# Performance work log

Hardware: AMD Instinct MI355X
Metric: run time of the kernel (lower is better)

Reference implementation:

```python
import jax, jax.numpy as jnp
import numpy as np


def setup_inputs() -> dict:
    key = jax.random.key(0)
    ks = jax.random.split(key, 7)
    B, T, U = 8, 200, 50
    D_enc, D_dec, J, V = 512, 512, 512, 1024
    s = 0.05
    return {
        "h_enc": jax.random.normal(ks[0], (B, T, 1, D_enc), dtype=jnp.float32),
        "h_dec": jax.random.normal(ks[1], (B, 1, U, D_dec), dtype=jnp.float32),
        "W_enc": jax.random.normal(ks[2], (J, D_enc), dtype=jnp.float32) * s,
        "b_enc": jax.random.normal(ks[3], (J,), dtype=jnp.float32) * s,
        "W_dec": jax.random.normal(ks[4], (J, D_dec), dtype=jnp.float32) * s,
        "W_out": jax.random.normal(ks[5], (V, J), dtype=jnp.float32) * s,
        "b_out": jax.random.normal(ks[6], (V,), dtype=jnp.float32) * s,
    }


def reference(h_enc, h_dec, W_enc, b_enc, W_dec, W_out, b_out):
    # lin_enc: (B,T,1,D_enc) -> (B,T,1,J) ; lin_dec (no bias): (B,1,U,D_dec) -> (B,1,U,J)
    e = jnp.einsum("btod,jd->btoj", h_enc, W_enc) + b_enc
    d = jnp.einsum("boud,jd->bouj", h_dec, W_dec)
    # broadcast add -> (B,T,U,J), Tanh activation
    z = jnp.tanh(e + d)
    # lin_out: (B,T,U,J) -> (B,T,U,V)
    return jnp.einsum("btuj,vj->btuv", z, W_out) + b_out
```

## Files before the change

kernel.cpp:

```cpp
#include <hip/hip_runtime.h>
#include <hip/hip_bf16.h>


typedef short bf16x8 __attribute__((ext_vector_type(8)));
typedef float fx4 __attribute__((ext_vector_type(4)));

static constexpr int KD = 512;
static constexpr int V = 1024;

__device__ inline unsigned short f2bf(float f) {
    union { float f; unsigned u; } v; v.f = f;
    unsigned r = v.u + 0x7fffu + ((v.u >> 16) & 1u);
    return (unsigned short)(r >> 16);
}
__device__ inline float bf2f(unsigned short h) {
    union { float f; unsigned u; } v; v.u = ((unsigned)h) << 16; return v.f;
}
__device__ inline float fast_tanh(float x) {
    float p = __builtin_amdgcn_exp2f(x * 2.885390081777926f);
    return 1.0f - 2.0f * __builtin_amdgcn_rcpf(p + 1.0f);
}
__device__ inline void gld_lds16(const void* g, void* l) {
    __builtin_amdgcn_global_load_lds(
        (const __attribute__((address_space(1))) void*)g,
        (__attribute__((address_space(3))) void*)l, 16, 0, 0);
}

__global__ __launch_bounds__(256) void prep(
    const float* __restrict__ h_enc, const float* __restrict__ W_enc,
    const float* __restrict__ b_enc, const float* __restrict__ h_dec,
    const float* __restrict__ W_dec, const float* __restrict__ W_out,
    float* __restrict__ e, float* __restrict__ dd, unsigned short* __restrict__ Wb) {
    const int bx = blockIdx.x;
    const int t = threadIdx.x;
    if (bx >= 256) {
        int i = ((bx - 256) * 256 + t) * 8;
        fx4 a = *(const fx4*)(W_out + i);
        fx4 b = *(const fx4*)(W_out + i + 4);
        unsigned short p[8];
        #pragma unroll
        for (int j = 0; j < 4; j++) { p[j] = f2bf(a[j]); p[j + 4] = f2bf(b[j]); }
        *(bf16x8*)(Wb + i) = *(bf16x8*)p;
        return;
    }
    const float* A; const float* W; const float* bias; float* out;
    int Mrows, mb, nb;
    if (bx < 200) { A = h_enc; W = W_enc; bias = b_enc; out = e;  Mrows = 1600; mb = bx >> 3; nb = bx & 7; }
    else { int b2 = bx - 200; A = h_dec; W = W_dec; bias = nullptr; out = dd; Mrows = 400; mb = b2 >> 3; nb = b2 & 7; }

    __shared__ unsigned short As[64 * 32];
    __shared__ unsigned short Ws[64 * 32];
    const int lane = t & 63, wid = t >> 6;
    const int m0 = mb * 64, n0 = nb * 64;
    const int wm = (wid & 1) * 32, wn = (wid >> 1) * 32;

    fx4 acc[2][2];
    const fx4 z4 = {0.f, 0.f, 0.f, 0.f};
    acc[0][0] = z4; acc[0][1] = z4; acc[1][0] = z4; acc[1][1] = z4;

    const int sr = t >> 2;
    const int skc = (t & 3) * 8;
    const int ar = (m0 + sr < Mrows) ? (m0 + sr) : (Mrows - 1);
    const float* Ap = A + (size_t)ar * KD + skc;
    const float* Wp = W + (size_t)(n0 + sr) * KD + skc;
    unsigned short* asl = &As[sr * 32 + skc];
    unsigned short* wsl = &Ws[sr * 32 + skc];

    for (int ph = 0; ph < 2; ph++) {
        const int wmode = (ph == 1);
        for (int kb = 0; kb < 16; kb++) {
            const int k0 = kb * 32;
            fx4 a0 = *(const fx4*)(Ap + k0);
            fx4 a1 = *(const fx4*)(Ap + k0 + 4);
            fx4 w0 = *(const fx4*)(Wp + k0);
            fx4 w1 = *(const fx4*)(Wp + k0 + 4);
            unsigned short pa[8], pw[8];
            #pragma unroll
            for (int i = 0; i < 4; i++) {
                unsigned short h;
                pa[i] = f2bf(a0[i]); pa[i + 4] = f2bf(a1[i]);
                h = f2bf(w0[i]); pw[i]     = wmode ? f2bf(w0[i] - bf2f(h)) : h;
                h = f2bf(w1[i]); pw[i + 4] = wmode ? f2bf(w1[i] - bf2f(h)) : h;
            }
            *(bf16x8*)asl = *(bf16x8*)pa;
            *(bf16x8*)wsl = *(bf16x8*)pw;
            __syncthreads();
            bf16x8 af[2], wf[2];
            #pragma unroll
            for (int f = 0; f < 2; f++) {
                af[f] = *(const bf16x8*)&As[(wm + f * 16 + (lane & 15)) * 32 + (lane >> 4) * 8];
                wf[f] = *(const bf16x8*)&Ws[(wn + f * 16 + (lane & 15)) * 32 + (lane >> 4) * 8];
            }
            #pragma unroll
            for (int fm = 0; fm < 2; fm++)
                #pragma unroll
                for (int fn = 0; fn < 2; fn++)
                    acc[fm][fn] = __builtin_amdgcn_mfma_f32_16x16x32_bf16(
                        af[fm], wf[fn], acc[fm][fn], 0, 0, 0);
            __syncthreads();
        }
    }
    const int colb = n0 + wn + (lane & 15);
    const int rowb = m0 + wm + (lane >> 4) * 4;
    float bo[2];
    bo[0] = bias ? bias[colb] : 0.f;
    bo[1] = bias ? bias[colb + 16] : 0.f;
    #pragma unroll
    for (int fm = 0; fm < 2; fm++) {
        #pragma unroll
        for (int r = 0; r < 4; r++) {
            int row = rowb + fm * 16 + r;
            if (row < Mrows) {
                float* op = out + (size_t)row * KD;
                op[colb] = acc[fm][0][r] + bo[0];
                op[colb + 16] = acc[fm][1][r] + bo[1];
            }
        }
    }
}

__global__ __launch_bounds__(256) void tanh_z(
    const float* __restrict__ e, const float* __restrict__ d,
    unsigned short* __restrict__ Z) {
    const int t = threadIdx.x;
    const int m = blockIdx.x * 4 + (t >> 6);
    const int kc = (t & 63) * 8;
    const int bt = m / 50;
    const int u = m - bt * 50;
    const int b = m / 10000;
    const float* ep = e + (size_t)bt * KD + kc;
    const float* dp = d + (size_t)(b * 50 + u) * KD + kc;
    fx4 e0 = *(const fx4*)ep, e1 = *(const fx4*)(ep + 4);
    fx4 d0 = *(const fx4*)dp, d1 = *(const fx4*)(dp + 4);
    unsigned short p[8];
    #pragma unroll
    for (int i = 0; i < 4; i++) {
        p[i] = f2bf(fast_tanh(e0[i] + d0[i]));
        p[i + 4] = f2bf(fast_tanh(e1[i] + d1[i]));
    }
    *(bf16x8*)(Z + (size_t)m * KD + kc) = *(bf16x8*)p;
}

__global__ __launch_bounds__(512, 2) void gemm_out_k8(
    const unsigned short* __restrict__ Z, const unsigned short* __restrict__ Wb,
    const float* __restrict__ b_out, float* __restrict__ out) {
    __shared__ unsigned short As[2][2][256 * 32];
    __shared__ unsigned short Bs[2][2][256 * 32];
    const int t = threadIdx.x;
    const int lane = t & 63, wid = t >> 6;
    const int bid = blockIdx.x;
    const int n0 = (bid & 3) * 256;
    const int m0 = (bid >> 2) * 256;
    const int wm = (wid >> 2) * 128;
    const int wn = (wid & 3) * 64;

    fx4 acc[8][4];
    const fx4 z4 = {0.f, 0.f, 0.f, 0.f};
    #pragma unroll
    for (int i = 0; i < 8; i++)
        #pragma unroll
        for (int j = 0; j < 4; j++) acc[i][j] = z4;

    size_t gA[2], gB[2];
    int lb[2];
    #pragma unroll
    for (int q = 0; q < 2; q++) {
        int rl = (wid * 2 + q) * 16 + (lane >> 2);
        int kc = (lane & 3) * 8;
        int ra = m0 + rl; if (ra > 79999) ra = 79999;
        gA[q] = (size_t)ra * KD + kc;
        gB[q] = (size_t)(n0 + rl) * KD + kc;
        lb[q] = (wid * 2 + q) * 512;
    }

    const int offA = (wm + (lane & 15)) * 32 + (lane >> 4) * 8;
    const int offB = (wn + (lane & 15)) * 32 + (lane >> 4) * 8;

    gld_lds16(Z + gA[0], &As[0][0][lb[0]]);
    gld_lds16(Z + gA[1], &As[0][0][lb[1]]);
    gld_lds16(Wb + gB[0], &Bs[0][0][lb[0]]);
    gld_lds16(Wb + gB[1], &Bs[0][0][lb[1]]);
    gld_lds16(Z + gA[0] + 32, &As[0][1][lb[0]]);
    gld_lds16(Z + gA[1] + 32, &As[0][1][lb[1]]);
    gld_lds16(Wb + gB[0] + 32, &Bs[0][1][lb[0]]);
    gld_lds16(Wb + gB[1] + 32, &Bs[0][1][lb[1]]);
    asm volatile("s_waitcnt vmcnt(4)" ::: "memory");
    __builtin_amdgcn_s_barrier();

    #pragma unroll 2
    for (int kt = 0; kt < 8; kt++) {
        const int cb = kt & 1, cb2 = cb ^ 1;
        const size_t ko = (size_t)(kt + 1) * 64;
        const bool pf = (kt < 7);
        bf16x8 afA[4], afB[4], bfA[4];

        #pragma unroll
        for (int i = 0; i < 4; i++) afA[i] = *(const bf16x8*)&As[cb][0][offA + i * 512];
        #pragma unroll
        for (int i = 0; i < 4; i++) bfA[i] = *(const bf16x8*)&Bs[cb][0][offB + i * 512];
        if (pf) {
            gld_lds16(Z + gA[0] + ko, &As[cb2][0][lb[0]]);
            gld_lds16(Z + gA[1] + ko, &As[cb2][0][lb[1]]);
        }
        __builtin_amdgcn_s_barrier();
        asm volatile("s_waitcnt lgkmcnt(0)" ::: "memory");
        __builtin_amdgcn_sched_barrier(0);
        __builtin_amdgcn_s_setprio(1);
        #pragma unroll
        for (int m = 0; m < 4; m++)
            #pragma unroll
            for (int n = 0; n < 4; n++)
                acc[m][n] = __builtin_amdgcn_mfma_f32_16x16x32_bf16(afA[m], bfA[n], acc[m][n], 0, 0, 0);
        __builtin_amdgcn_s_setprio(0);
        __builtin_amdgcn_s_barrier();

        #pragma unroll
        for (int i = 0; i < 4; i++) afB[i] = *(const bf16x8*)&As[cb][0][offA + (4 + i) * 512];
        if (pf) {
            gld_lds16(Wb + gB[0] + ko, &Bs[cb2][0][lb[0]]);
            gld_lds16(Wb + gB[1] + ko, &Bs[cb2][0][lb[1]]);
            asm volatile("s_waitcnt vmcnt(4)" ::: "memory");
        } else {
            asm volatile("s_waitcnt vmcnt(0)" ::: "memory");
        }
        __builtin_amdgcn_s_barrier();
        asm volatile("s_waitcnt lgkmcnt(0)" ::: "memory");
        __builtin_amdgcn_sched_barrier(0);
        __builtin_amdgcn_s_setprio(1);
        #pragma unroll
        for (int m = 0; m < 4; m++)
            #pragma unroll
            for (int n = 0; n < 4; n++)
                acc[4 + m][n] = __builtin_amdgcn_mfma_f32_16x16x32_bf16(afB[m], bfA[n], acc[4 + m][n], 0, 0, 0);
        __builtin_amdgcn_s_setprio(0);
        __builtin_amdgcn_s_barrier();

        #pragma unroll
        for (int i = 0; i < 4; i++) afA[i] = *(const bf16x8*)&As[cb][1][offA + i * 512];
        #pragma unroll
        for (int i = 0; i < 4; i++) bfA[i] = *(const bf16x8*)&Bs[cb][1][offB + i * 512];
        if (pf) {
            gld_lds16(Z + gA[0] + ko + 32, &As[cb2][1][lb[0]]);
            gld_lds16(Z + gA[1] + ko + 32, &As[cb2][1][lb[1]]);
        }
        __builtin_amdgcn_s_barrier();
        asm volatile("s_waitcnt lgkmcnt(0)" ::: "memory");
        __builtin_amdgcn_sched_barrier(0);
        __builtin_amdgcn_s_setprio(1);
        #pragma unroll
        for (int m = 0; m < 4; m++)
            #pragma unroll
            for (int n = 0; n < 4; n++)
                acc[m][n] = __builtin_amdgcn_mfma_f32_16x16x32_bf16(afA[m], bfA[n], acc[m][n], 0, 0, 0);
        __builtin_amdgcn_s_setprio(0);
        __builtin_amdgcn_s_barrier();

        #pragma unroll
        for (int i = 0; i < 4; i++) afB[i] = *(const bf16x8*)&As[cb][1][offA + (4 + i) * 512];
        if (pf) {
            gld_lds16(Wb + gB[0] + ko + 32, &Bs[cb2][1][lb[0]]);
            gld_lds16(Wb + gB[1] + ko + 32, &Bs[cb2][1][lb[1]]);
            asm volatile("s_waitcnt vmcnt(4)" ::: "memory");
        }
        __builtin_amdgcn_s_barrier();
        asm volatile("s_waitcnt lgkmcnt(0)" ::: "memory");
        __builtin_amdgcn_sched_barrier(0);
        __builtin_amdgcn_s_setprio(1);
        #pragma unroll
        for (int m = 0; m < 4; m++)
            #pragma unroll
            for (int n = 0; n < 4; n++)
                acc[4 + m][n] = __builtin_amdgcn_mfma_f32_16x16x32_bf16(afB[m], bfA[n], acc[4 + m][n], 0, 0, 0);
        __builtin_amdgcn_s_setprio(0);
        __builtin_amdgcn_s_barrier();
    }

    const int colb = n0 + wn + (lane & 15);
    const int rowb = m0 + wm + (lane >> 4) * 4;
    float bo[4];
    #pragma unroll
    for (int fn = 0; fn < 4; fn++) bo[fn] = b_out[colb + fn * 16];
    #pragma unroll
    for (int fm = 0; fm < 8; fm++) {
        #pragma unroll
        for (int r = 0; r < 4; r++) {
            const int row = rowb + fm * 16 + r;
            if (row < 80000) {
                float* op = out + (size_t)row * V;
                #pragma unroll
                for (int fn = 0; fn < 4; fn++)
                    op[colb + fn * 16] = acc[fm][fn][r] + bo[fn];
            }
        }
    }
}

extern "C" void kernel_launch(void* const* d_in, const int* in_sizes, int n_in,
                              void* d_out, int out_size, void* d_ws, size_t ws_size,
                              hipStream_t stream) {
    const float* h_enc = (const float*)d_in[0];
    const float* h_dec = (const float*)d_in[1];
    const float* W_enc = (const float*)d_in[2];
    const float* b_enc = (const float*)d_in[3];
    const float* W_dec = (const float*)d_in[4];
    const float* W_out = (const float*)d_in[5];
    const float* b_out = (const float*)d_in[6];
    float* out = (float*)d_out;

    float* e = (float*)d_ws;
    float* dd = e + 1600 * KD;
    unsigned short* Wb = (unsigned short*)(dd + 400 * KD);
    unsigned short* Zb = Wb + (size_t)V * KD;

    prep<<<512, 256, 0, stream>>>(h_enc, W_enc, b_enc, h_dec, W_dec, W_out, e, dd, Wb);
    tanh_z<<<20000, 256, 0, stream>>>(e, dd, Zb);
    gemm_out_k8<<<313 * 4, 512, 0, stream>>>(Zb, Wb, b_out, out);
}
```

Measured before the change: 455.0 us.

## Fuse tanh(e+d) activation into output GEMM A-tile loading

Removes the separate tanh_z kernel and its bf16 Z intermediate. The GEMM now loads fp32 e and d rows into registers, computes tanh, converts to bf16 and writes the A tile into LDS itself, while W_out tiles still use direct global-to-LDS loads. This avoids the Z write and reread traffic and one launch. In exchange, tanh is recomputed once per N-block (4x), and it adds VALU and register pressure inside the MFMA pipeline.

```diff
diff --git a/kernel.cpp b/kernel.cpp
--- a/kernel.cpp
+++ b/kernel.cpp
@@ -119,30 +119,9 @@
     }
 }
 
-__global__ __launch_bounds__(256) void tanh_z(
-    const float* __restrict__ e, const float* __restrict__ d,
-    unsigned short* __restrict__ Z) {
-    const int t = threadIdx.x;
-    const int m = blockIdx.x * 4 + (t >> 6);
-    const int kc = (t & 63) * 8;
-    const int bt = m / 50;
-    const int u = m - bt * 50;
-    const int b = m / 10000;
-    const float* ep = e + (size_t)bt * KD + kc;
-    const float* dp = d + (size_t)(b * 50 + u) * KD + kc;
-    fx4 e0 = *(const fx4*)ep, e1 = *(const fx4*)(ep + 4);
-    fx4 d0 = *(const fx4*)dp, d1 = *(const fx4*)(dp + 4);
-    unsigned short p[8];
-    #pragma unroll
-    for (int i = 0; i < 4; i++) {
-        p[i] = f2bf(fast_tanh(e0[i] + d0[i]));
-        p[i + 4] = f2bf(fast_tanh(e1[i] + d1[i]));
-    }
-    *(bf16x8*)(Z + (size_t)m * KD + kc) = *(bf16x8*)p;
-}
-
-__global__ __launch_bounds__(512, 2) void gemm_out_k8(
-    const unsigned short* __restrict__ Z, const unsigned short* __restrict__ Wb,
+__global__ __launch_bounds__(512, 2) void gemm_fused(
+    const float* __restrict__ e, const float* __restrict__ dd,
+    const unsigned short* __restrict__ Wb,
     const float* __restrict__ b_out, float* __restrict__ out) {
     __shared__ unsigned short As[2][2][256 * 32];
     __shared__ unsigned short Bs[2][2][256 * 32];
@@ -161,36 +140,70 @@
         #pragma unroll
         for (int j = 0; j < 4; j++) acc[i][j] = z4;
 
-    size_t gA[2], gB[2];
+    const int kc = (lane & 3) * 8;
+    unsigned eo[2], dof[2], gBo[2];
     int lb[2];
     #pragma unroll
     for (int q = 0; q < 2; q++) {
         int rl = (wid * 2 + q) * 16 + (lane >> 2);
-        int kc = (lane & 3) * 8;
-        int ra = m0 + rl; if (ra > 79999) ra = 79999;
-        gA[q] = (size_t)ra * KD + kc;
-        gB[q] = (size_t)(n0 + rl) * KD + kc;
-        lb[q] = (wid * 2 + q) * 512;
+        int m = m0 + rl; if (m > 79999) m = 79999;
+        int bt = m / 50;
+        int b  = m / 10000;
+        int u  = m - bt * 50;
+        eo[q]  = (unsigned)bt * KD + kc;
+        dof[q] = (unsigned)(b * 50 + u) * KD + kc;
+        gBo[q] = (unsigned)(n0 + rl) * KD + kc;
+        lb[q]  = (wid * 2 + q) * 512;
     }
 
     const int offA = (wm + (lane & 15)) * 32 + (lane >> 4) * 8;
     const int offB = (wn + (lane & 15)) * 32 + (lane >> 4) * 8;
 
-    gld_lds16(Z + gA[0], &As[0][0][lb[0]]);
-    gld_lds16(Z + gA[1], &As[0][0][lb[1]]);
-    gld_lds16(Wb + gB[0], &Bs[0][0][lb[0]]);
-    gld_lds16(Wb + gB[1], &Bs[0][0][lb[1]]);
-    gld_lds16(Z + gA[0] + 32, &As[0][1][lb[0]]);
-    gld_lds16(Z + gA[1] + 32, &As[0][1][lb[1]]);
-    gld_lds16(Wb + gB[0] + 32, &Bs[0][1][lb[0]]);
-    gld_lds16(Wb + gB[1] + 32, &Bs[0][1][lb[1]]);
-    asm volatile("s_waitcnt vmcnt(4)" ::: "memory");
+    fx4 se0[2], se1[2], sd0[2], sd1[2];
+
+    #pragma unroll
+    for (int q = 0; q < 2; q++) {
+        se0[q] = *(const fx4*)(e + eo[q]);      se1[q] = *(const fx4*)(e + eo[q] + 4);
+        sd0[q] = *(const fx4*)(dd + dof[q]);    sd1[q] = *(const fx4*)(dd + dof[q] + 4);
+    }
+    gld_lds16(Wb + gBo[0], &Bs[0][0][lb[0]]);
+    gld_lds16(Wb + gBo[1], &Bs[0][0][lb[1]]);
+    asm volatile("s_waitcnt vmcnt(2)" ::: "memory");
+    #pragma unroll
+    for (int q = 0; q < 2; q++) {
+        unsigned short p[8];
+        #pragma unroll
+        for (int i = 0; i < 4; i++) {
+            p[i]     = f2bf(fast_tanh(se0[q][i] + sd0[q][i]));
+            p[i + 4] = f2bf(fast_tanh(se1[q][i] + sd1[q][i]));
+        }
+        *(bf16x8*)&As[0][0][lb[q] + lane * 8] = *(bf16x8*)p;
+    }
+    #pragma unroll
+    for (int q = 0; q < 2; q++) {
+        se0[q] = *(const fx4*)(e + eo[q] + 32);   se1[q] = *(const fx4*)(e + eo[q] + 36);
+        sd0[q] = *(const fx4*)(dd + dof[q] + 32); sd1[q] = *(const fx4*)(dd + dof[q] + 36);
+    }
+    gld_lds16(Wb + gBo[0] + 32, &Bs[0][1][lb[0]]);
+    gld_lds16(Wb + gBo[1] + 32, &Bs[0][1][lb[1]]);
+    asm volatile("s_waitcnt vmcnt(2)" ::: "memory");
+    #pragma unroll
+    for (int q = 0; q < 2; q++) {
+        unsigned short p[8];
+        #pragma unroll
+        for (int i = 0; i < 4; i++) {
+            p[i]     = f2bf(fast_tanh(se0[q][i] + sd0[q][i]));
+            p[i + 4] = f2bf(fast_tanh(se1[q][i] + sd1[q][i]));
+        }
+        *(bf16x8*)&As[0][1][lb[q] + lane * 8] = *(bf16x8*)p;
+    }
+    asm volatile("s_waitcnt lgkmcnt(0)" ::: "memory");
     __builtin_amdgcn_s_barrier();
 
     #pragma unroll 2
     for (int kt = 0; kt < 8; kt++) {
         const int cb = kt & 1, cb2 = cb ^ 1;
-        const size_t ko = (size_t)(kt + 1) * 64;
+        const unsigned ko = (unsigned)(kt + 1) * 64;
         const bool pf = (kt < 7);
         bf16x8 afA[4], afB[4], bfA[4];
 
@@ -199,8 +212,11 @@
         #pragma unroll
         for (int i = 0; i < 4; i++) bfA[i] = *(const bf16x8*)&Bs[cb][0][offB + i * 512];
         if (pf) {
-            gld_lds16(Z + gA[0] + ko, &As[cb2][0][lb[0]]);
-            gld_lds16(Z + gA[1] + ko, &As[cb2][0][lb[1]]);
+            #pragma unroll
+            for (int q = 0; q < 2; q++) {
+                se0[q] = *(const fx4*)(e + eo[q] + ko);      se1[q] = *(const fx4*)(e + eo[q] + ko + 4);
+                sd0[q] = *(const fx4*)(dd + dof[q] + ko);    sd1[q] = *(const fx4*)(dd + dof[q] + ko + 4);
+            }
         }
         __builtin_amdgcn_s_barrier();
         asm volatile("s_waitcnt lgkmcnt(0)" ::: "memory");
@@ -217,9 +233,19 @@
         #pragma unroll
         for (int i = 0; i < 4; i++) afB[i] = *(const bf16x8*)&As[cb][0][offA + (4 + i) * 512];
         if (pf) {
-            gld_lds16(Wb + gB[0] + ko, &Bs[cb2][0][lb[0]]);
-            gld_lds16(Wb + gB[1] + ko, &Bs[cb2][0][lb[1]]);
-            asm volatile("s_waitcnt vmcnt(4)" ::: "memory");
+            gld_lds16(Wb + gBo[0] + ko, &Bs[cb2][0][lb[0]]);
+            gld_lds16(Wb + gBo[1] + ko, &Bs[cb2][0][lb[1]]);
+            asm volatile("s_waitcnt vmcnt(2)" ::: "memory");
+            #pragma unroll
+            for (int q = 0; q < 2; q++) {
+                unsigned short p[8];
+                #pragma unroll
+                for (int i = 0; i < 4; i++) {
+                    p[i]     = f2bf(fast_tanh(se0[q][i] + sd0[q][i]));
+                    p[i + 4] = f2bf(fast_tanh(se1[q][i] + sd1[q][i]));
+                }
+                *(bf16x8*)&As[cb2][0][lb[q] + lane * 8] = *(bf16x8*)p;
+            }
         } else {
             asm volatile("s_waitcnt vmcnt(0)" ::: "memory");
         }
@@ -240,8 +266,13 @@
         #pragma unroll
         for (int i = 0; i < 4; i++) bfA[i] = *(const bf16x8*)&Bs[cb][1][offB + i * 512];
         if (pf) {
-            gld_lds16(Z + gA[0] + ko + 32, &As[cb2][1][lb[0]]);
-            gld_lds16(Z + gA[1] + ko + 32, &As[cb2][1][lb[1]]);
+            #pragma unroll
+            for (int q = 0; q < 2; q++) {
+                se0[q] = *(const fx4*)(e + eo[q] + ko + 32);   se1[q] = *(const fx4*)(e + eo[q] + ko + 36);
+                sd0[q] = *(const fx4*)(dd + dof[q] + ko + 32); sd1[q] = *(const fx4*)(dd + dof[q] + ko + 36);
+            }
+            gld_lds16(Wb + gBo[0] + ko + 32, &Bs[cb2][1][lb[0]]);
+            gld_lds16(Wb + gBo[1] + ko + 32, &Bs[cb2][1][lb[1]]);
         }
         __builtin_amdgcn_s_barrier();
         asm volatile("s_waitcnt lgkmcnt(0)" ::: "memory");
@@ -258,9 +289,17 @@
         #pragma unroll
         for (int i = 0; i < 4; i++) afB[i] = *(const bf16x8*)&As[cb][1][offA + (4 + i) * 512];
         if (pf) {
-            gld_lds16(Wb + gB[0] + ko + 32, &Bs[cb2][1][lb[0]]);
-            gld_lds16(Wb + gB[1] + ko + 32, &Bs[cb2][1][lb[1]]);
-            asm volatile("s_waitcnt vmcnt(4)" ::: "memory");
+            asm volatile("s_waitcnt vmcnt(2)" ::: "memory");
+            #pragma unroll
+            for (int q = 0; q < 2; q++) {
+                unsigned short p[8];
+                #pragma unroll
+                for (int i = 0; i < 4; i++) {
+                    p[i]     = f2bf(fast_tanh(se0[q][i] + sd0[q][i]));
+                    p[i + 4] = f2bf(fast_tanh(se1[q][i] + sd1[q][i]));
+                }
+                *(bf16x8*)&As[cb2][1][lb[q] + lane * 8] = *(bf16x8*)p;
+            }
         }
         __builtin_amdgcn_s_barrier();
         asm volatile("s_waitcnt lgkmcnt(0)" ::: "memory");
@@ -310,9 +349,7 @@
     float* e = (float*)d_ws;
     float* dd = e + 1600 * KD;
     unsigned short* Wb = (unsigned short*)(dd + 400 * KD);
-    unsigned short* Zb = Wb + (size_t)V * KD;
 
     prep<<<512, 256, 0, stream>>>(h_enc, W_enc, b_enc, h_dec, W_dec, W_out, e, dd, Wb);
-    tanh_z<<<20000, 256, 0, stream>>>(e, dd, Zb);
-    gemm_out_k8<<<313 * 4, 512, 0, stream>>>(Zb, Wb, b_out, out);
-}
+    gemm_fused<<<313 * 4, 512, 0, stream>>>(e, dd, Wb, b_out, out);
+}
```

After: 555.9 us. 1.22x slower.
